# Kernel tuning notes

Measured on AMD Instinct MI355X. Metric: run time of the kernel, lower is better.

Reference implementation:

```python
import jax, jax.numpy as jnp
import numpy as np
from jax import lax

B, N, C, HEADS, SR = 2, 4096, 256, 8, 2
HW = 64

def setup_inputs() -> dict:
    key = jax.random.key(0)
    ks = jax.random.split(key, 12)
    s = 0.02
    return {
        "x0": jax.random.normal(ks[0], (B, N, C), jnp.float32),
        "x1": jax.random.normal(ks[1], (B, N, C), jnp.float32),
        "Wq": jax.random.normal(ks[2], (C, C), jnp.float32) * s,
        "Wkv": jax.random.normal(ks[3], (2 * C, C), jnp.float32) * s,
        "Wproj": jax.random.normal(ks[4], (C, C), jnp.float32) * s,
        "bproj": jnp.zeros((C,), jnp.float32),
        "Wsr": jax.random.normal(ks[5], (C, C, SR, SR), jnp.float32) * np.sqrt(2.0 / (SR * SR * C)),
        "bsr": jnp.zeros((C,), jnp.float32),
        "ln_w0": jnp.ones((C,), jnp.float32),
        "ln_b0": jnp.zeros((C,), jnp.float32),
        "ln_w1": jnp.ones((C,), jnp.float32),
        "ln_b1": jnp.zeros((C,), jnp.float32),
        "H": HW,
        "W": HW,
    }

def _layernorm(x, w, b, eps=1e-5):
    mu = jnp.mean(x, axis=-1, keepdims=True)
    var = jnp.mean(jnp.square(x - mu), axis=-1, keepdims=True)
    return (x - mu) * lax.rsqrt(var + eps) * w + b

def _attend(x, ln_w, ln_b, Wq, Wkv, Wproj, bproj, Wsr, bsr, H, W):
    b, n, c = x.shape
    h = HEADS
    d = c // h
    scale = d ** -0.5
    # q: (B, h, N, d)
    q = (x @ Wq.T).reshape(b, n, h, d).transpose(0, 2, 1, 3)
    # spatial reduction: conv k=stride=sr on (B,C,H,W)
    xs = x.transpose(0, 2, 1).reshape(b, c, H, W)
    xs = lax.conv_general_dilated(xs, Wsr, (SR, SR), 'VALID',
                                  dimension_numbers=('NCHW', 'OIHW', 'NCHW'))
    xs = xs + bsr[None, :, None, None]
    m = (H // SR) * (W // SR)
    xs = xs.reshape(b, c, m).transpose(0, 2, 1)  # (B, M, C)
    xs = _layernorm(xs, ln_w, ln_b)
    kv = (xs @ Wkv.T).reshape(b, m, 2, h, d).transpose(2, 0, 3, 1, 4)
    k, v = kv[0], kv[1]  # (B, h, M, d)
    attn = jnp.einsum('bhnd,bhmd->bhnm', q, k) * scale
    attn = jax.nn.softmax(attn, axis=-1)
    out = jnp.einsum('bhnm,bhmd->bhnd', attn, v)
    out = out.transpose(0, 2, 1, 3).reshape(b, n, c)
    return out @ Wproj.T + bproj

def reference(x0, x1, Wq, Wkv, Wproj, bproj, Wsr, bsr, ln_w0, ln_b0, ln_w1, ln_b1, H, W):
    y0 = _attend(x0, ln_w0, ln_b0, Wq, Wkv, Wproj, bproj, Wsr, bsr, H, W)
    y1 = _attend(x1, ln_w1, ln_b1, Wq, Wkv, Wproj, bproj, Wsr, bsr, H, W)
    return (y0, y1)
```

## Files before the change

kernel.cpp:

```cpp
#include <hip/hip_runtime.h>
#include <hip/hip_bf16.h>
#include <cstddef>

typedef __hip_bfloat16 bf16;
typedef __attribute__((ext_vector_type(8))) short bf16x8;
typedef __attribute__((ext_vector_type(4))) float f32x4;
typedef __attribute__((ext_vector_type(4))) short short4v;

__device__ __forceinline__ float b2f(bf16 v) { return __bfloat162float(v); }
__device__ __forceinline__ bf16 f2b(float v) { return __float2bfloat16(v); }

#define MFMA(a, b, c) __builtin_amdgcn_mfma_f32_16x16x32_bf16((a), (b), (c), 0, 0, 0)

#define WQ_OFF   0
#define WKV_OFF  65536
#define WP_OFF   196608
#define WSR_OFF  262144

__global__ __launch_bounds__(256) void prep_cvt(
    const float* __restrict__ x0, const float* __restrict__ x1,
    bf16* __restrict__ xb,
    const float* __restrict__ Wq, const float* __restrict__ Wkv,
    const float* __restrict__ Wp, const float* __restrict__ Wsr,
    bf16* __restrict__ wb) {
  const int t = threadIdx.x;
  if (blockIdx.x < 1024) {
    const int gid = blockIdx.x * 256 + t;
    for (int i = gid; i < 1048576; i += 262144) {
      const float4 v = (i < 524288) ? ((const float4*)x0)[i]
                                    : ((const float4*)x1)[i - 524288];
      union { bf16 h[4]; short4v s; } u;
      u.h[0] = f2b(v.x); u.h[1] = f2b(v.y); u.h[2] = f2b(v.z); u.h[3] = f2b(v.w);
      ((short4v*)xb)[i] = u.s;
    }
  } else {
    const int gid = (blockIdx.x - 1024) * 256 + t;
    for (int i = gid; i < 524288; i += 131072) {
      float v;
      if (i < WKV_OFF)       v = Wq[i];
      else if (i < WP_OFF)   v = Wkv[i - WKV_OFF];
      else if (i < WSR_OFF)  v = Wp[i - WP_OFF];
      else {
        const int r = i - WSR_OFF;
        const int o = r >> 10, k = r & 1023;
        const int p = k >> 8, c = k & 255;
        v = Wsr[o * 1024 + c * 4 + p];
      }
      wb[i] = f2b(v);
    }
  }
}

#define STAGE_W(W_lds, wgl, ldg)                                             \
  _Pragma("unroll")                                                          \
  for (int u = 0; u < 8; ++u) {                                              \
    const int idx = u * 256 + t;                                             \
    const int wr = idx >> 5;                                                 \
    const int wc = (idx & 31) * 8;                                           \
    *(bf16x8*)&W_lds[wr][wc] = *(const bf16x8*)((wgl) + wr * (ldg) + wc);    \
  }

__global__ __launch_bounds__(256) void qc_mfma(
    const bf16* __restrict__ xb, const bf16* __restrict__ wb,
    const float* __restrict__ bsr, bf16* __restrict__ q,
    bf16* __restrict__ xsb) {
  __shared__ bf16 W_lds[64][264];
  const int t = threadIdx.x;
  const int wave = t >> 6, lane = t & 63, quad = lane >> 4, l16 = lane & 15;
  const int colh = blockIdx.y * 64;

  if (blockIdx.x < 256) {
    const int row0 = blockIdx.x * 64 + wave * 16;
    STAGE_W(W_lds, wb + WQ_OFF + colh * 256, 256);
    __syncthreads();
    const bf16* ap = xb + (row0 + l16) * 256 + quad * 8;
    f32x4 acc[4];
    #pragma unroll
    for (int j = 0; j < 4; ++j) acc[j] = (f32x4){0.f, 0.f, 0.f, 0.f};
    #pragma unroll
    for (int k0 = 0; k0 < 256; k0 += 32) {
      const bf16x8 af = *(const bf16x8*)(ap + k0);
      #pragma unroll
      for (int j = 0; j < 4; ++j) {
        const bf16x8 wf = *(const bf16x8*)&W_lds[j * 16 + l16][k0 + quad * 8];
        acc[j] = MFMA(af, wf, acc[j]);
      }
    }
    const float scale = 0.2550348572f;
    #pragma unroll
    for (int j = 0; j < 4; ++j)
      #pragma unroll
      for (int r = 0; r < 4; ++r)
        q[(row0 + quad * 4 + r) * 256 + colh + j * 16 + l16] =
            f2b(acc[j][r] * scale);
  } else {
    const int bx = blockIdx.x - 256;
    const int row0 = bx * 64 + wave * 16;
    const int mrow = row0 + l16;
    const int ab = mrow >> 10;
    const int m = mrow & 1023;
    const int mi_ = m >> 5, mj = m & 31;
    f32x4 acc[4];
    #pragma unroll
    for (int j = 0; j < 4; ++j) acc[j] = (f32x4){0.f, 0.f, 0.f, 0.f};
    for (int p = 0; p < 4; ++p) {
      __syncthreads();
      STAGE_W(W_lds, wb + WSR_OFF + colh * 1024 + p * 256, 1024);
      __syncthreads();
      const int n = (2 * mi_ + (p >> 1)) * 64 + 2 * mj + (p & 1);
      const bf16* ap = xb + (ab * 4096 + n) * 256 + quad * 8;
      #pragma unroll
      for (int c0 = 0; c0 < 256; c0 += 32) {
        const bf16x8 af = *(const bf16x8*)(ap + c0);
        #pragma unroll
        for (int j = 0; j < 4; ++j) {
          const bf16x8 wf = *(const bf16x8*)&W_lds[j * 16 + l16][c0 + quad * 8];
          acc[j] = MFMA(af, wf, acc[j]);
        }
      }
    }
    #pragma unroll
    for (int j = 0; j < 4; ++j) {
      const int col = colh + j * 16 + l16;
      const float bv = bsr[col];
      #pragma unroll
      for (int r = 0; r < 4; ++r)
        xsb[(row0 + quad * 4 + r) * 256 + col] = f2b(acc[j][r] + bv);
    }
  }
}

__global__ __launch_bounds__(256) void kvln_mfma(
    const bf16* __restrict__ xsb, const bf16* __restrict__ wb,
    const float* __restrict__ w0, const float* __restrict__ b0,
    const float* __restrict__ w1, const float* __restrict__ b1,
    bf16* __restrict__ kbuf, bf16* __restrict__ vbuf_t) {
  __shared__ bf16 W_lds[64][264];
  __shared__ float lnw[256], lnb[256];
  const int t = threadIdx.x;
  const int wave = t >> 6, lane = t & 63, quad = lane >> 4, l16 = lane & 15;
  const int row0 = blockIdx.x * 64 + wave * 16;
  const int colh = blockIdx.y * 64;
  const int a = (blockIdx.x * 64) >> 11;
  lnw[t] = a ? w1[t] : w0[t];
  lnb[t] = a ? b1[t] : b0[t];
  STAGE_W(W_lds, wb + WKV_OFF + colh * 256, 256);
  __syncthreads();

  const bf16* ap = xsb + (row0 + l16) * 256 + quad * 8;
  bf16x8 af[8];
  float sum = 0.f, ss = 0.f;
  #pragma unroll
  for (int i = 0; i < 8; ++i) {
    af[i] = *(const bf16x8*)(ap + i * 32);
    #pragma unroll
    for (int e = 0; e < 8; ++e) {
      const float x = b2f(((bf16*)&af[i])[e]);
      sum += x; ss += x * x;
    }
  }
  sum += __shfl_xor(sum, 16, 64); sum += __shfl_xor(sum, 32, 64);
  ss  += __shfl_xor(ss, 16, 64);  ss  += __shfl_xor(ss, 32, 64);
  const float mu = sum * (1.0f / 256.0f);
  const float var = ss * (1.0f / 256.0f) - mu * mu;
  const float rstd = rsqrtf(var + 1e-5f);
  #pragma unroll
  for (int i = 0; i < 8; ++i) {
    const int cb = i * 32 + quad * 8;
    union { bf16 h[8]; bf16x8 v; } u;
    #pragma unroll
    for (int e = 0; e < 8; ++e) {
      const float x = b2f(((bf16*)&af[i])[e]);
      u.h[e] = f2b((x - mu) * rstd * lnw[cb + e] + lnb[cb + e]);
    }
    af[i] = u.v;
  }

  f32x4 acc[4];
  #pragma unroll
  for (int j = 0; j < 4; ++j) acc[j] = (f32x4){0.f, 0.f, 0.f, 0.f};
  #pragma unroll
  for (int i = 0; i < 8; ++i) {
    #pragma unroll
    for (int j = 0; j < 4; ++j) {
      const bf16x8 wf = *(const bf16x8*)&W_lds[j * 16 + l16][i * 32 + quad * 8];
      acc[j] = MFMA(af[i], wf, acc[j]);
    }
  }
  #pragma unroll
  for (int j = 0; j < 4; ++j) {
    const int o = colh + j * 16 + l16;
    #pragma unroll
    for (int r = 0; r < 4; ++r) {
      const int row = row0 + quad * 4 + r;
      const int m = row & 1023;
      const bf16 val = f2b(acc[j][r]);
      if (o < 256) {
        const int h = o >> 5, d = o & 31;
        kbuf[((row >> 10) * 8 + h) * 32768 + m * 32 + d] = val;
      } else {
        const int o2 = o - 256;
        const int h = o2 >> 5, d = o2 & 31;
        const int rr = m & 63;
        const int mp = (m & ~63) + (rr & 15) * 4 + (rr >> 4);
        vbuf_t[((row >> 10) * 8 + h) * 32768 + d * 1024 + mp] = val;
      }
    }
  }
}

__global__ __launch_bounds__(256) void attn_mfma(
    const bf16* __restrict__ q, const bf16* __restrict__ kbuf,
    const bf16* __restrict__ vbuf_t, bf16* __restrict__ att) {
  const int abh = blockIdx.y;
  const int ab = abh >> 3;
  const int h = abh & 7;
  const int t = threadIdx.x;
  const int wave = t >> 6, lane = t & 63, quad = lane >> 4, l16 = lane & 15;
  const int qbase = blockIdx.x * 128 + wave * 32;

  __shared__ bf16 KT[2][2048];
  __shared__ bf16 VT[2][2048];
  __shared__ bf16 P_lds[4][2][16][72];

  const bf16* kb = kbuf + abh * 32768;
  const bf16* vb = vbuf_t + abh * 32768;

  const int kg = (t >> 6) * 512 + ((t >> 2) & 15) * 32 + (t & 3) * 8;
  const int vg_row = (t >> 7) * 16 + ((t >> 3) & 15);
  const int vg_col = ((t >> 2) & 1) * 32 + (t & 3) * 8;

  bf16x8 qf[2];
  #pragma unroll
  for (int s = 0; s < 2; ++s)
    qf[s] = *(const bf16x8*)(
        q + (ab * 4096 + qbase + s * 16 + l16) * 256 + h * 32 + quad * 8);

  {
    const bf16x8 kr = *(const bf16x8*)(kb + kg);
    const bf16x8 vr = *(const bf16x8*)(vb + vg_row * 1024 + vg_col);
    *(bf16x8*)&KT[0][t * 8] = kr;
    *(bf16x8*)&VT[0][t * 8] = vr;
  }
  __syncthreads();

  f32x4 o[2][2];
  float lp[2][4];
  #pragma unroll
  for (int s = 0; s < 2; ++s) {
    o[s][0] = (f32x4){0.f, 0.f, 0.f, 0.f};
    o[s][1] = (f32x4){0.f, 0.f, 0.f, 0.f};
    #pragma unroll
    for (int r = 0; r < 4; ++r) lp[s][r] = 0.0f;
  }
  const f32x4 zero = {0.f, 0.f, 0.f, 0.f};

  for (int kt = 0; kt < 16; ++kt) {
    const int cur = kt & 1;
    bf16x8 kr, vr;
    const bool pf = (kt + 1 < 16);
    if (pf) {
      const int nk0 = (kt + 1) * 64;
      kr = *(const bf16x8*)(kb + nk0 * 32 + kg);
      vr = *(const bf16x8*)(vb + vg_row * 1024 + nk0 + vg_col);
    }
    f32x4 S[2][4];
    #pragma unroll
    for (int tt = 0; tt < 4; ++tt) {
      const bf16x8 kf =
          *(const bf16x8*)&KT[cur][(tt * 64 + l16 * 4 + quad) * 8];
      S[0][tt] = MFMA(qf[0], kf, zero);
      S[1][tt] = MFMA(qf[1], kf, zero);
    }
    #pragma unroll
    for (int s = 0; s < 2; ++s) {
      #pragma unroll
      for (int r = 0; r < 4; ++r) {
        const float p0 = __builtin_amdgcn_exp2f(S[s][0][r]);
        const float p1 = __builtin_amdgcn_exp2f(S[s][1][r]);
        const float p2 = __builtin_amdgcn_exp2f(S[s][2][r]);
        const float p3 = __builtin_amdgcn_exp2f(S[s][3][r]);
        lp[s][r] += (p0 + p1) + (p2 + p3);
        const __hip_bfloat162 lo = __float22bfloat162_rn(float2{p0, p1});
        const __hip_bfloat162 hi = __float22bfloat162_rn(float2{p2, p3});
        union { __hip_bfloat162 h2[2]; short4v sv; } u;
        u.h2[0] = lo; u.h2[1] = hi;
        *(short4v*)&P_lds[wave][s][quad * 4 + r][l16 * 4] = u.sv;
      }
    }
    #pragma unroll
    for (int c2 = 0; c2 < 2; ++c2) {
      const bf16x8 pf0 = *(const bf16x8*)&P_lds[wave][0][l16][c2 * 32 + quad * 8];
      const bf16x8 pf1 = *(const bf16x8*)&P_lds[wave][1][l16][c2 * 32 + quad * 8];
      #pragma unroll
      for (int dh = 0; dh < 2; ++dh) {
        const bf16x8 vf = *(const bf16x8*)&VT[cur]
            [(dh * 128 + l16 * 8 + c2 * 4 + quad) * 8];
        o[0][dh] = MFMA(pf0, vf, o[0][dh]);
        o[1][dh] = MFMA(pf1, vf, o[1][dh]);
      }
    }
    if (pf) {
      *(bf16x8*)&KT[cur ^ 1][t * 8] = kr;
      *(bf16x8*)&VT[cur ^ 1][t * 8] = vr;
    }
    __syncthreads();
  }
  #pragma unroll
  for (int s = 0; s < 2; ++s) {
    #pragma unroll
    for (int r = 0; r < 4; ++r) {
      float li = lp[s][r];
      #pragma unroll
      for (int off = 1; off < 16; off <<= 1) li += __shfl_xor(li, off, 16);
      const float inv = 1.0f / li;
      const int qrow = ab * 4096 + qbase + s * 16 + quad * 4 + r;
      bf16* orow = att + qrow * 256 + h * 32;
      orow[l16]      = f2b(o[s][0][r] * inv);
      orow[16 + l16] = f2b(o[s][1][r] * inv);
    }
  }
}

__global__ __launch_bounds__(256) void proj_mfma(
    const bf16* __restrict__ att, const bf16* __restrict__ wb,
    const float* __restrict__ bp, float* __restrict__ outp) {
  __shared__ bf16 W_lds[64][264];
  const int t = threadIdx.x;
  const int wave = t >> 6, lane = t & 63, quad = lane >> 4, l16 = lane & 15;
  const int row0 = blockIdx.x * 64 + wave * 16;
  const int colh = blockIdx.y * 64;
  STAGE_W(W_lds, wb + WP_OFF + colh * 256, 256);
  __syncthreads();
  const bf16* ap = att + (row0 + l16) * 256 + quad * 8;
  f32x4 acc[4];
  #pragma unroll
  for (int j = 0; j < 4; ++j) acc[j] = (f32x4){0.f, 0.f, 0.f, 0.f};
  #pragma unroll
  for (int k0 = 0; k0 < 256; k0 += 32) {
    const bf16x8 af = *(const bf16x8*)(ap + k0);
    #pragma unroll
    for (int j = 0; j < 4; ++j) {
      const bf16x8 wf = *(const bf16x8*)&W_lds[j * 16 + l16][k0 + quad * 8];
      acc[j] = MFMA(af, wf, acc[j]);
    }
  }
  #pragma unroll
  for (int j = 0; j < 4; ++j) {
    const int col = colh + j * 16 + l16;
    const float bv = bp[col];
    #pragma unroll
    for (int r = 0; r < 4; ++r)
      outp[(row0 + quad * 4 + r) * 256 + col] = acc[j][r] + bv;
  }
}

extern "C" void kernel_launch(void* const* d_in, const int* in_sizes, int n_in,
                              void* d_out, int out_size, void* d_ws, size_t ws_size,
                              hipStream_t stream) {
  const float* x0    = (const float*)d_in[0];
  const float* x1    = (const float*)d_in[1];
  const float* Wq    = (const float*)d_in[2];
  const float* Wkv   = (const float*)d_in[3];
  const float* Wproj = (const float*)d_in[4];
  const float* bproj = (const float*)d_in[5];
  const float* Wsr   = (const float*)d_in[6];
  const float* bsr   = (const float*)d_in[7];
  const float* lnw0  = (const float*)d_in[8];
  const float* lnb0  = (const float*)d_in[9];
  const float* lnw1  = (const float*)d_in[10];
  const float* lnb1  = (const float*)d_in[11];

  bf16* q_bf   = (bf16*)d_out;
  bf16* xb     = q_bf + 4194304;
  bf16* att_bf = (bf16*)d_ws;
  bf16* xsb    = att_bf + 4194304;
  bf16* kbuf   = xsb + 1048576;
  bf16* vbuf_t = kbuf + 1048576;
  bf16* wb     = vbuf_t + 1048576;
  float* y     = (float*)d_out;

  const dim3 blk(256);
  prep_cvt<<<dim3(1536), blk, 0, stream>>>(x0, x1, xb, Wq, Wkv, Wproj, Wsr, wb);
  qc_mfma<<<dim3(320, 4), blk, 0, stream>>>(xb, wb, bsr, q_bf, xsb);
  kvln_mfma<<<dim3(64, 8), blk, 0, stream>>>(xsb, wb, lnw0, lnb0, lnw1, lnb1,
                                             kbuf, vbuf_t);
  attn_mfma<<<dim3(32, 32), blk, 0, stream>>>(q_bf, kbuf, vbuf_t, att_bf);
  proj_mfma<<<dim3(256, 4), blk, 0, stream>>>(att_bf, wb, bproj, y);
}
```

Measured before the change: 160.8 us.

## Keep attention probabilities in registers by transposing the QK MFMA

Swaps the operands of the QK^T MFMA so each lane holds scores for one query column, which lets the exp'd probabilities be packed directly into the A-operand layout of the PV MFMA without a round trip through LDS. The V buffer permutation written by the KV kernel is changed to match the new key ordering within each 64-key tile. Row sums are now accumulated per lane and reduced with cross-quad shuffles at the end, then broadcast per output row. This removes per-tile LDS writes and reads of P and the associated LDS traffic, at the cost of correctness depending on the permuted V layout matching the register layout exactly.

```diff
diff --git a/kernel.cpp b/kernel.cpp
--- a/kernel.cpp
+++ b/kernel.cpp
@@ -202,7 +202,8 @@
         const int o2 = o - 256;
         const int h = o2 >> 5, d = o2 & 31;
         const int rr = m & 63;
-        const int mp = (m & ~63) + (rr & 15) * 4 + (rr >> 4);
+        const int mp = (m & ~63) | (rr & 32) | ((rr & 12) << 1) |
+                       ((rr & 16) >> 2) | (rr & 3);
         vbuf_t[((row >> 10) * 8 + h) * 32768 + d * 1024 + mp] = val;
       }
     }
@@ -216,12 +217,11 @@
   const int ab = abh >> 3;
   const int h = abh & 7;
   const int t = threadIdx.x;
-  const int wave = t >> 6, lane = t & 63, quad = lane >> 4, l16 = lane & 15;
-  const int qbase = blockIdx.x * 128 + wave * 32;
+  const int lane = t & 63, quad = lane >> 4, l16 = lane & 15;
+  const int qbase = blockIdx.x * 128 + (t >> 6) * 32;
 
   __shared__ bf16 KT[2][2048];
   __shared__ bf16 VT[2][2048];
-  __shared__ bf16 P_lds[4][2][16][72];
 
   const bf16* kb = kbuf + abh * 32768;
   const bf16* vb = vbuf_t + abh * 32768;
@@ -245,13 +245,11 @@
   __syncthreads();
 
   f32x4 o[2][2];
-  float lp[2][4];
+  float lp[2] = {0.f, 0.f};
   #pragma unroll
   for (int s = 0; s < 2; ++s) {
     o[s][0] = (f32x4){0.f, 0.f, 0.f, 0.f};
     o[s][1] = (f32x4){0.f, 0.f, 0.f, 0.f};
-    #pragma unroll
-    for (int r = 0; r < 4; ++r) lp[s][r] = 0.0f;
   }
   const f32x4 zero = {0.f, 0.f, 0.f, 0.f};
 
@@ -269,35 +267,40 @@
     for (int tt = 0; tt < 4; ++tt) {
       const bf16x8 kf =
           *(const bf16x8*)&KT[cur][(tt * 64 + l16 * 4 + quad) * 8];
-      S[0][tt] = MFMA(qf[0], kf, zero);
-      S[1][tt] = MFMA(qf[1], kf, zero);
-    }
+      S[0][tt] = MFMA(kf, qf[0], zero);
+      S[1][tt] = MFMA(kf, qf[1], zero);
+    }
+    bf16x8 pa[2][2];
     #pragma unroll
     for (int s = 0; s < 2; ++s) {
-      #pragma unroll
-      for (int r = 0; r < 4; ++r) {
-        const float p0 = __builtin_amdgcn_exp2f(S[s][0][r]);
-        const float p1 = __builtin_amdgcn_exp2f(S[s][1][r]);
-        const float p2 = __builtin_amdgcn_exp2f(S[s][2][r]);
-        const float p3 = __builtin_amdgcn_exp2f(S[s][3][r]);
-        lp[s][r] += (p0 + p1) + (p2 + p3);
-        const __hip_bfloat162 lo = __float22bfloat162_rn(float2{p0, p1});
-        const __hip_bfloat162 hi = __float22bfloat162_rn(float2{p2, p3});
-        union { __hip_bfloat162 h2[2]; short4v sv; } u;
-        u.h2[0] = lo; u.h2[1] = hi;
-        *(short4v*)&P_lds[wave][s][quad * 4 + r][l16 * 4] = u.sv;
+      float p[4][4];
+      float acc = 0.f;
+      #pragma unroll
+      for (int tt = 0; tt < 4; ++tt)
+        #pragma unroll
+        for (int r = 0; r < 4; ++r) {
+          p[tt][r] = __builtin_amdgcn_exp2f(S[s][tt][r]);
+          acc += p[tt][r];
+        }
+      lp[s] += acc;
+      #pragma unroll
+      for (int c2 = 0; c2 < 2; ++c2) {
+        union { __hip_bfloat162 h2[4]; bf16x8 v; } u;
+        u.h2[0] = __float22bfloat162_rn(float2{p[c2 * 2][0], p[c2 * 2][1]});
+        u.h2[1] = __float22bfloat162_rn(float2{p[c2 * 2][2], p[c2 * 2][3]});
+        u.h2[2] = __float22bfloat162_rn(float2{p[c2 * 2 + 1][0], p[c2 * 2 + 1][1]});
+        u.h2[3] = __float22bfloat162_rn(float2{p[c2 * 2 + 1][2], p[c2 * 2 + 1][3]});
+        pa[s][c2] = u.v;
       }
     }
     #pragma unroll
     for (int c2 = 0; c2 < 2; ++c2) {
-      const bf16x8 pf0 = *(const bf16x8*)&P_lds[wave][0][l16][c2 * 32 + quad * 8];
-      const bf16x8 pf1 = *(const bf16x8*)&P_lds[wave][1][l16][c2 * 32 + quad * 8];
       #pragma unroll
       for (int dh = 0; dh < 2; ++dh) {
         const bf16x8 vf = *(const bf16x8*)&VT[cur]
             [(dh * 128 + l16 * 8 + c2 * 4 + quad) * 8];
-        o[0][dh] = MFMA(pf0, vf, o[0][dh]);
-        o[1][dh] = MFMA(pf1, vf, o[1][dh]);
+        o[0][dh] = MFMA(pa[0][c2], vf, o[0][dh]);
+        o[1][dh] = MFMA(pa[1][c2], vf, o[1][dh]);
       }
     }
     if (pf) {
@@ -308,11 +311,14 @@
   }
   #pragma unroll
   for (int s = 0; s < 2; ++s) {
+    lp[s] += __shfl_xor(lp[s], 16, 64);
+    lp[s] += __shfl_xor(lp[s], 32, 64);
+  }
+  #pragma unroll
+  for (int s = 0; s < 2; ++s) {
     #pragma unroll
     for (int r = 0; r < 4; ++r) {
-      float li = lp[s][r];
-      #pragma unroll
-      for (int off = 1; off < 16; off <<= 1) li += __shfl_xor(li, off, 16);
+      const float li = __shfl(lp[s], quad * 4 + r, 16);
       const float inv = 1.0f / li;
       const int qrow = ab * 4096 + qbase + s * 16 + quad * 4 + r;
       bf16* orow = att + qrow * 256 + h * 32;
```

Result: no change. 158.8 us (-1.2%).
